# Optimization experiments

Measured on AMD Instinct MI355X. Metric: run time of the kernel, lower is better.

Reference implementation:

```python
import jax, jax.numpy as jnp
import numpy as np

B, T, C = 1, 2048, 2048
N_HEADS, N_KV_HEADS = 32, 8
D_HEAD = C // N_HEADS  # 64
WINDOW = 512
ROPE_BASE = 10000.0


def setup_inputs() -> dict:
    key = jax.random.key(0)
    ks = jax.random.split(key, 5)
    s = 0.02
    return {
        "x": jax.random.normal(ks[0], (B, T, C), dtype=jnp.float32),
        "wq": jax.random.normal(ks[1], (C, N_HEADS * D_HEAD), dtype=jnp.float32) * s,
        "wk": jax.random.normal(ks[2], (C, N_KV_HEADS * D_HEAD), dtype=jnp.float32) * s,
        "wv": jax.random.normal(ks[3], (C, N_KV_HEADS * D_HEAD), dtype=jnp.float32) * s,
        "wo": jax.random.normal(ks[4], (N_HEADS * D_HEAD, C), dtype=jnp.float32) * s,
    }


def _rope_tables(seq_len, d_head, dtype):
    inv_freq = 1.0 / (ROPE_BASE ** (jnp.arange(0, d_head, 2, dtype=jnp.float32) / d_head))
    t = jnp.arange(seq_len, dtype=jnp.float32)
    freqs = t[:, None] * inv_freq[None, :]          # [T, d/2]
    emb = jnp.concatenate([freqs, freqs], axis=-1)  # [T, d]
    return jnp.cos(emb).astype(dtype), jnp.sin(emb).astype(dtype)


def _rotate_half(u):
    d = u.shape[-1]
    return jnp.concatenate([-u[..., d // 2:], u[..., :d // 2]], axis=-1)


def reference(x, wq, wk, wv, wo):
    b, t, c = x.shape
    n_rep = N_HEADS // N_KV_HEADS
    q = (x @ wq).reshape(b, t, N_HEADS, D_HEAD)
    k = (x @ wk).reshape(b, t, N_KV_HEADS, D_HEAD)
    v = (x @ wv).reshape(b, t, N_KV_HEADS, D_HEAD)

    cos, sin = _rope_tables(t, D_HEAD, x.dtype)
    cos = cos[None, :, None, :]
    sin = sin[None, :, None, :]
    q = q * cos + _rotate_half(q) * sin
    k = k * cos + _rotate_half(k) * sin

    # repeat_interleave KV heads up to n_heads (GQA expansion)
    k = jnp.repeat(k, n_rep, axis=2)  # [B,T,H,d]
    v = jnp.repeat(v, n_rep, axis=2)

    scale = 1.0 / np.sqrt(D_HEAD)
    scores = jnp.einsum('bqhd,bkhd->bhqk', q, k) * scale  # [B,H,T,T]

    # sliding-window causal mask: attend iff k<=q and q-k<=window
    qi = jnp.arange(t)[:, None]
    ki = jnp.arange(t)[None, :]
    allowed = (ki <= qi) & (qi - ki <= WINDOW)  # [T,T] bool
    scores = jnp.where(allowed[None, None, :, :], scores, -jnp.inf)

    attn = jax.nn.softmax(scores, axis=-1)
    out = jnp.einsum('bhqk,bkhd->bqhd', attn, v).reshape(b, t, N_HEADS * D_HEAD)
    return out @ wo
```

## Files before the change

### kernel.cpp

```cpp
#include <hip/hip_runtime.h>
#include <hip/hip_bf16.h>
#include <math.h>

#define T_SEQ 2048
#define C_DIM 2048
#define NH    32
#define NKV   8
#define DH    64
#define WIN   512
#define QKV_N 3072

typedef __bf16 bf16x8 __attribute__((ext_vector_type(8)));
typedef __bf16 bf16x4 __attribute__((ext_vector_type(4)));
typedef float  f32x4  __attribute__((ext_vector_type(4)));

__device__ __forceinline__ void gload_lds16(const __bf16* g, __bf16* l) {
  __builtin_amdgcn_global_load_lds(
      (const __attribute__((address_space(1))) void*)g,
      (__attribute__((address_space(3))) void*)l, 16, 0, 0);
}

__device__ __forceinline__ void tr_tile(const float* __restrict__ in,
                                        __bf16* __restrict__ out,
                                        int R, int Ccols, int tile, int tid,
                                        float (*sh)[33]) {
  int tpc = Ccols >> 5;
  int c0 = (tile % tpc) << 5;
  int r0 = (tile / tpc) << 5;
  int tx = tid & 31, ty = tid >> 5;
#pragma unroll
  for (int i = 0; i < 32; i += 8)
    sh[ty + i][tx] = in[(size_t)(r0 + ty + i) * Ccols + c0 + tx];
  __syncthreads();
#pragma unroll
  for (int i = 0; i < 32; i += 8)
    out[(size_t)(c0 + ty + i) * R + r0 + tx] = (__bf16)sh[tx][ty + i];
}

__global__ __launch_bounds__(256) void prep_kernel(
    const float* __restrict__ x, const float* __restrict__ wq,
    const float* __restrict__ wk, const float* __restrict__ wv,
    const float* __restrict__ wo, __bf16* __restrict__ xb,
    __bf16* __restrict__ wqkvT, __bf16* __restrict__ woT,
    float2* __restrict__ tab) {
  __shared__ float sh[32][33];
  int bid = blockIdx.x;
  const int tid = threadIdx.x;
  if (bid < 4096) {
    int i = bid * 256 + tid;
    float4 v = ((const float4*)x)[i];
    bf16x4 o = {(__bf16)v.x, (__bf16)v.y, (__bf16)v.z, (__bf16)v.w};
    *(bf16x4*)(xb + (size_t)i * 4) = o;
    return;
  }
  bid -= 4096;
  if (bid < 256) {
    int i = bid * 256 + tid;
    int j = i & 31, t = i >> 5;
    float inv = powf(10000.0f, -(float)(2 * j) / 64.0f);
    float s, c;
    sincosf((float)t * inv, &s, &c);
    tab[i] = make_float2(c, s);
    return;
  }
  bid -= 256;
  if (bid < 4096) { tr_tile(wq, wqkvT, C_DIM, C_DIM, bid, tid, sh); return; }
  bid -= 4096;
  if (bid < 1024) {
    tr_tile(wk, wqkvT + (size_t)2048 * C_DIM, C_DIM, NKV * DH, bid, tid, sh);
    return;
  }
  bid -= 1024;
  if (bid < 1024) {
    tr_tile(wv, wqkvT + (size_t)2560 * C_DIM, C_DIM, NKV * DH, bid, tid, sh);
    return;
  }
  bid -= 1024;
  tr_tile(wo, woT, C_DIM, C_DIM, bid, tid, sh);
}

template <typename OutT, bool ROPE>
__global__ __launch_bounds__(256) void gemm_bf16_kernel(
    const __bf16* __restrict__ A, const __bf16* __restrict__ Bt,
    OutT* __restrict__ C, const float2* __restrict__ rope_tab,
    int M, int N, int K) {
  __shared__ __bf16 As[2][128 * 64];
  __shared__ __bf16 Bs[2][64 * 64];

  const int tid = threadIdx.x;
  const int wid = tid >> 6, l = tid & 63;
  const int lm = l & 15, lh = l >> 4;
  const int brow = blockIdx.y * 128, bcol = blockIdx.x * 64;

  const int kb_swz = (((l & 7) ^ (l >> 3)) << 3);
  const int srow   = l >> 3;

  f32x4 acc[2][4] = {};
  const int NT = K >> 6;

#pragma unroll
  for (int c = 0; c < 6; ++c) {
    int ci = wid + c * 4;
    if (ci < 16) {
      int row = ci * 8 + srow;
      gload_lds16(A + (size_t)(brow + row) * K + kb_swz, &As[0][ci * 512]);
    } else {
      int row = (ci - 16) * 8 + srow;
      gload_lds16(Bt + (size_t)(bcol + row) * K + kb_swz, &Bs[0][(ci - 16) * 512]);
    }
  }
  __syncthreads();

  for (int t = 0; t < NT; ++t) {
    const int cur = t & 1;
    if (t + 1 < NT) {
      const int k1 = (t + 1) << 6;
#pragma unroll
      for (int c = 0; c < 6; ++c) {
        int ci = wid + c * 4;
        if (ci < 16) {
          int row = ci * 8 + srow;
          gload_lds16(A + (size_t)(brow + row) * K + k1 + kb_swz,
                      &As[cur ^ 1][ci * 512]);
        } else {
          int row = (ci - 16) * 8 + srow;
          gload_lds16(Bt + (size_t)(bcol + row) * K + k1 + kb_swz,
                      &Bs[cur ^ 1][(ci - 16) * 512]);
        }
      }
    }

    const __bf16* as = As[cur];
    const __bf16* bs = Bs[cur];
    const int x7 = lm & 7;
    bf16x8 af[2][2], bfr[4][2];
#pragma unroll
    for (int i = 0; i < 2; ++i)
#pragma unroll
      for (int u = 0; u < 2; ++u)
        af[i][u] = *(const bf16x8*)&as[(wid * 32 + i * 16 + lm) * 64 +
                                       (((u * 4 + lh) ^ x7) << 3)];
#pragma unroll
    for (int j = 0; j < 4; ++j)
#pragma unroll
      for (int u = 0; u < 2; ++u)
        bfr[j][u] = *(const bf16x8*)&bs[(j * 16 + lm) * 64 +
                                        (((u * 4 + lh) ^ x7) << 3)];
#pragma unroll
    for (int u = 0; u < 2; ++u)
#pragma unroll
      for (int i = 0; i < 2; ++i)
#pragma unroll
        for (int j = 0; j < 4; ++j)
          acc[i][j] = __builtin_amdgcn_mfma_f32_16x16x32_bf16(
              af[i][u], bfr[j][u], acc[i][j], 0, 0, 0);

    __syncthreads();
  }

  if (ROPE) {
    if (bcol < 2560) {
#pragma unroll
      for (int i = 0; i < 2; ++i)
#pragma unroll
        for (int r = 0; r < 4; ++r) {
          int t = brow + wid * 32 + i * 16 + lh * 4 + r;
#pragma unroll
          for (int j = 0; j < 2; ++j) {
            float2 cs = rope_tab[t * 32 + j * 16 + lm];
            float v0 = acc[i][j][r], v1 = acc[i][j + 2][r];
            acc[i][j][r]     = v0 * cs.x - v1 * cs.y;
            acc[i][j + 2][r] = v1 * cs.x + v0 * cs.y;
          }
        }
    }
  }

#pragma unroll
  for (int i = 0; i < 2; ++i)
#pragma unroll
    for (int j = 0; j < 4; ++j)
#pragma unroll
      for (int r = 0; r < 4; ++r) {
        int row = brow + wid * 32 + i * 16 + lh * 4 + r;
        int col = bcol + j * 16 + lm;
        C[(size_t)row * N + col] = (OutT)acc[i][j][r];
      }
}

__global__ __launch_bounds__(256) void attn_mfma_kernel(
    const __bf16* __restrict__ QKV, __bf16* __restrict__ O) {
  __shared__ __bf16 K_lds[64][72];
  __shared__ __bf16 Vt[64][72];
  __shared__ __bf16 P_lds[4][16][72];

  const int tid = threadIdx.x;
  const int l   = tid & 63;
  const int w   = tid >> 6;
  const int q0  = blockIdx.x * 64;
  const int h   = blockIdx.y;
  const int kvh = h >> 2;
  const int q0w = q0 + w * 16;
  const int lm  = l & 15;
  const int lh  = l >> 4;

  const __bf16* Qp = QKV + h * DH;
  const __bf16* Kp = QKV + 2048 + kvh * DH;
  const __bf16* Vp = QKV + 2560 + kvh * DH;

  bf16x8 aq0 = *(const bf16x8*)(Qp + (size_t)(q0w + lm) * QKV_N + lh * 8);
  bf16x8 aq1 = *(const bf16x8*)(Qp + (size_t)(q0w + lm) * QKV_N + 32 + lh * 8);

  f32x4 o_acc[4] = {};
  float m[4], lsum[4];
#pragma unroll
  for (int r = 0; r < 4; ++r) { m[r] = -1e30f; lsum[r] = 0.0f; }

  const int klo  = (q0 - WIN) > 0 ? (q0 - WIN) : 0;
  const int skey = tid >> 2;
  const int sdp  = (tid & 3) * 16;

  for (int k0 = klo; k0 < q0 + 64; k0 += 64) {
    __syncthreads();
    {
      const __bf16* ks = Kp + (size_t)(k0 + skey) * QKV_N + sdp;
      *(bf16x8*)&K_lds[skey][sdp]     = *(const bf16x8*)ks;
      *(bf16x8*)&K_lds[skey][sdp + 8] = *(const bf16x8*)(ks + 8);
      const __bf16* vs = Vp + (size_t)(k0 + l) * QKV_N + w * 16;
      bf16x8 v0 = *(const bf16x8*)vs;
      bf16x8 v1 = *(const bf16x8*)(vs + 8);
#pragma unroll
      for (int j = 0; j < 8; ++j) Vt[w * 16 + j][l]     = v0[j];
#pragma unroll
      for (int j = 0; j < 8; ++j) Vt[w * 16 + 8 + j][l] = v1[j];
    }
    __syncthreads();

    f32x4 s[4] = {};
#pragma unroll
    for (int kg = 0; kg < 4; ++kg) {
      bf16x8 kb0 = *(const bf16x8*)&K_lds[kg * 16 + lm][lh * 8];
      bf16x8 kb1 = *(const bf16x8*)&K_lds[kg * 16 + lm][32 + lh * 8];
      s[kg] = __builtin_amdgcn_mfma_f32_16x16x32_bf16(aq0, kb0, s[kg], 0, 0, 0);
      s[kg] = __builtin_amdgcn_mfma_f32_16x16x32_bf16(aq1, kb1, s[kg], 0, 0, 0);
    }

    float sv[4][4];
    float tmax[4] = {-1e30f, -1e30f, -1e30f, -1e30f};
#pragma unroll
    for (int kg = 0; kg < 4; ++kg)
#pragma unroll
      for (int r = 0; r < 4; ++r) {
        int qr = q0w + lh * 4 + r;
        int kc = k0 + kg * 16 + lm;
        float a = s[kg][r] * 0.125f;
        sv[kg][r] = (kc <= qr && kc + WIN >= qr) ? a : -1e30f;
        tmax[r] = fmaxf(tmax[r], sv[kg][r]);
      }
#pragma unroll
    for (int off = 1; off < 16; off <<= 1)
#pragma unroll
      for (int r = 0; r < 4; ++r)
        tmax[r] = fmaxf(tmax[r], __shfl_xor(tmax[r], off));

#pragma unroll
    for (int r = 0; r < 4; ++r) {
      float mn = fmaxf(m[r], tmax[r]);
      float co = __expf(m[r] - mn);
      m[r] = mn;
      float ps = 0.0f;
#pragma unroll
      for (int kg = 0; kg < 4; ++kg) {
        float p = (sv[kg][r] > -1e29f) ? __expf(sv[kg][r] - mn) : 0.0f;
        sv[kg][r] = p;
        ps += p;
      }
#pragma unroll
      for (int off = 1; off < 16; off <<= 1) ps += __shfl_xor(ps, off);
      lsum[r] = lsum[r] * co + ps;
#pragma unroll
      for (int dc = 0; dc < 4; ++dc) o_acc[dc][r] *= co;
    }

#pragma unroll
    for (int kg = 0; kg < 4; ++kg)
#pragma unroll
      for (int r = 0; r < 4; ++r)
        P_lds[w][lh * 4 + r][kg * 16 + lm] = (__bf16)sv[kg][r];
    bf16x8 pf0 = *(const bf16x8*)&P_lds[w][lm][lh * 8];
    bf16x8 pf1 = *(const bf16x8*)&P_lds[w][lm][32 + lh * 8];

#pragma unroll
    for (int dc = 0; dc < 4; ++dc) {
      bf16x8 vb0 = *(const bf16x8*)&Vt[dc * 16 + lm][lh * 8];
      bf16x8 vb1 = *(const bf16x8*)&Vt[dc * 16 + lm][32 + lh * 8];
      o_acc[dc] = __builtin_amdgcn_mfma_f32_16x16x32_bf16(pf0, vb0, o_acc[dc], 0, 0, 0);
      o_acc[dc] = __builtin_amdgcn_mfma_f32_16x16x32_bf16(pf1, vb1, o_acc[dc], 0, 0, 0);
    }
  }

#pragma unroll
  for (int dc = 0; dc < 4; ++dc)
#pragma unroll
    for (int r = 0; r < 4; ++r) {
      int qr = q0w + lh * 4 + r;
      O[(size_t)qr * C_DIM + h * DH + dc * 16 + lm] =
          (__bf16)(o_acc[dc][r] / lsum[r]);
    }
}

extern "C" void kernel_launch(void* const* d_in, const int* in_sizes, int n_in,
                              void* d_out, int out_size, void* d_ws, size_t ws_size,
                              hipStream_t stream) {
  const float* x  = (const float*)d_in[0];
  const float* wq = (const float*)d_in[1];
  const float* wk = (const float*)d_in[2];
  const float* wv = (const float*)d_in[3];
  const float* wo = (const float*)d_in[4];
  float* out = (float*)d_out;

  __bf16* xb    = (__bf16*)d_ws;
  __bf16* wqkvT = xb + (size_t)C_DIM * C_DIM;
  __bf16* woT   = wqkvT + (size_t)QKV_N * C_DIM;
  __bf16* QKV   = woT + (size_t)C_DIM * C_DIM;
  float2* tab   = (float2*)(QKV + (size_t)T_SEQ * QKV_N);
  __bf16* Ab    = xb;

  prep_kernel<<<4096 + 256 + 4096 + 1024 + 1024 + 4096, 256, 0, stream>>>(
      x, wq, wk, wv, wo, xb, wqkvT, woT, tab);

  gemm_bf16_kernel<__bf16, true>
      <<<dim3(QKV_N / 64, T_SEQ / 128), 256, 0, stream>>>(
          xb, wqkvT, QKV, tab, T_SEQ, QKV_N, C_DIM);

  attn_mfma_kernel<<<dim3(T_SEQ / 64, NH), dim3(256), 0, stream>>>(QKV, Ab);

  gemm_bf16_kernel<float, false>
      <<<dim3(C_DIM / 64, T_SEQ / 128), 256, 0, stream>>>(
          Ab, woT, out, nullptr, T_SEQ, C_DIM, C_DIM);
}
```

Baseline: 125.9 us.

## Transpose attention MFMAs, fold softmax scale into Q projection, use exp2

Swaps the MFMA operands so each lane holds a single query row, which removes the cross-lane shuffle reductions per row and lets the output be stored as packed bf16x4. The softmax scale and log2(e) are folded into Q in the projection epilogue so the attention loop can use a raw exp2. Mask evaluation is skipped for tiles lying fully inside the window. The running max now starts at -60, which relies on scores staying above that bound.

```diff
diff --git a/kernel.cpp b/kernel.cpp
--- a/kernel.cpp
+++ b/kernel.cpp
@@ -13,6 +13,12 @@
 typedef __bf16 bf16x8 __attribute__((ext_vector_type(8)));
 typedef __bf16 bf16x4 __attribute__((ext_vector_type(4)));
 typedef float  f32x4  __attribute__((ext_vector_type(4)));
+
+#if __has_builtin(__builtin_amdgcn_exp2f)
+#define EXP2(x) __builtin_amdgcn_exp2f(x)
+#else
+#define EXP2(x) exp2f(x)
+#endif
 
 __device__ __forceinline__ void gload_lds16(const __bf16* g, __bf16* l) {
   __builtin_amdgcn_global_load_lds(
@@ -174,6 +180,14 @@
           }
         }
     }
+    if (bcol < 2048) {
+#pragma unroll
+      for (int i = 0; i < 2; ++i)
+#pragma unroll
+        for (int j = 0; j < 4; ++j)
+#pragma unroll
+          for (int r = 0; r < 4; ++r) acc[i][j][r] *= 0.18033688f;
+    }
   }
 
 #pragma unroll
@@ -212,9 +226,7 @@
   bf16x8 aq1 = *(const bf16x8*)(Qp + (size_t)(q0w + lm) * QKV_N + 32 + lh * 8);
 
   f32x4 o_acc[4] = {};
-  float m[4], lsum[4];
-#pragma unroll
-  for (int r = 0; r < 4; ++r) { m[r] = -1e30f; lsum[r] = 0.0f; }
+  float m = -60.0f, lsum = 0.0f;
 
   const int klo  = (q0 - WIN) > 0 ? (q0 - WIN) : 0;
   const int skey = tid >> 2;
@@ -241,52 +253,61 @@
     for (int kg = 0; kg < 4; ++kg) {
       bf16x8 kb0 = *(const bf16x8*)&K_lds[kg * 16 + lm][lh * 8];
       bf16x8 kb1 = *(const bf16x8*)&K_lds[kg * 16 + lm][32 + lh * 8];
-      s[kg] = __builtin_amdgcn_mfma_f32_16x16x32_bf16(aq0, kb0, s[kg], 0, 0, 0);
-      s[kg] = __builtin_amdgcn_mfma_f32_16x16x32_bf16(aq1, kb1, s[kg], 0, 0, 0);
+      s[kg] = __builtin_amdgcn_mfma_f32_16x16x32_bf16(kb0, aq0, s[kg], 0, 0, 0);
+      s[kg] = __builtin_amdgcn_mfma_f32_16x16x32_bf16(kb1, aq1, s[kg], 0, 0, 0);
     }
 
     float sv[4][4];
-    float tmax[4] = {-1e30f, -1e30f, -1e30f, -1e30f};
+    const bool full = (k0 + 63 <= q0w) && (k0 >= q0w + 15 - WIN);
+    if (full) {
+#pragma unroll
+      for (int kg = 0; kg < 4; ++kg)
+#pragma unroll
+        for (int r = 0; r < 4; ++r) sv[kg][r] = s[kg][r];
+    } else {
+      const int qr = q0w + lm;
+#pragma unroll
+      for (int kg = 0; kg < 4; ++kg)
+#pragma unroll
+        for (int r = 0; r < 4; ++r) {
+          int kc = k0 + kg * 16 + lh * 4 + r;
+          sv[kg][r] = (kc <= qr && kc + WIN >= qr) ? s[kg][r] : -1e30f;
+        }
+    }
+
+    float t01 = fmaxf(fmaxf(fmaxf(sv[0][0], sv[0][1]), fmaxf(sv[0][2], sv[0][3])),
+                      fmaxf(fmaxf(sv[1][0], sv[1][1]), fmaxf(sv[1][2], sv[1][3])));
+    float t23 = fmaxf(fmaxf(fmaxf(sv[2][0], sv[2][1]), fmaxf(sv[2][2], sv[2][3])),
+                      fmaxf(fmaxf(sv[3][0], sv[3][1]), fmaxf(sv[3][2], sv[3][3])));
+    float tmax = fmaxf(t01, t23);
+    tmax = fmaxf(tmax, __shfl_xor(tmax, 16));
+    tmax = fmaxf(tmax, __shfl_xor(tmax, 32));
+
+    float mn = fmaxf(m, tmax);
+    float co = EXP2(m - mn);
+    m = mn;
+    float ps = 0.0f;
 #pragma unroll
     for (int kg = 0; kg < 4; ++kg)
 #pragma unroll
       for (int r = 0; r < 4; ++r) {
-        int qr = q0w + lh * 4 + r;
-        int kc = k0 + kg * 16 + lm;
-        float a = s[kg][r] * 0.125f;
-        sv[kg][r] = (kc <= qr && kc + WIN >= qr) ? a : -1e30f;
-        tmax[r] = fmaxf(tmax[r], sv[kg][r]);
-      }
-#pragma unroll
-    for (int off = 1; off < 16; off <<= 1)
-#pragma unroll
-      for (int r = 0; r < 4; ++r)
-        tmax[r] = fmaxf(tmax[r], __shfl_xor(tmax[r], off));
-
-#pragma unroll
-    for (int r = 0; r < 4; ++r) {
-      float mn = fmaxf(m[r], tmax[r]);
-      float co = __expf(m[r] - mn);
-      m[r] = mn;
-      float ps = 0.0f;
-#pragma unroll
-      for (int kg = 0; kg < 4; ++kg) {
-        float p = (sv[kg][r] > -1e29f) ? __expf(sv[kg][r] - mn) : 0.0f;
+        float p = EXP2(sv[kg][r] - mn);
         sv[kg][r] = p;
         ps += p;
       }
-#pragma unroll
-      for (int off = 1; off < 16; off <<= 1) ps += __shfl_xor(ps, off);
-      lsum[r] = lsum[r] * co + ps;
-#pragma unroll
-      for (int dc = 0; dc < 4; ++dc) o_acc[dc][r] *= co;
-    }
+    ps += __shfl_xor(ps, 16);
+    ps += __shfl_xor(ps, 32);
+    lsum = lsum * co + ps;
+#pragma unroll
+    for (int dc = 0; dc < 4; ++dc)
+#pragma unroll
+      for (int r = 0; r < 4; ++r) o_acc[dc][r] *= co;
 
 #pragma unroll
     for (int kg = 0; kg < 4; ++kg)
 #pragma unroll
       for (int r = 0; r < 4; ++r)
-        P_lds[w][lh * 4 + r][kg * 16 + lm] = (__bf16)sv[kg][r];
+        P_lds[w][lm][kg * 16 + lh * 4 + r] = (__bf16)sv[kg][r];
     bf16x8 pf0 = *(const bf16x8*)&P_lds[w][lm][lh * 8];
     bf16x8 pf1 = *(const bf16x8*)&P_lds[w][lm][32 + lh * 8];
 
@@ -294,19 +315,19 @@
     for (int dc = 0; dc < 4; ++dc) {
       bf16x8 vb0 = *(const bf16x8*)&Vt[dc * 16 + lm][lh * 8];
       bf16x8 vb1 = *(const bf16x8*)&Vt[dc * 16 + lm][32 + lh * 8];
-      o_acc[dc] = __builtin_amdgcn_mfma_f32_16x16x32_bf16(pf0, vb0, o_acc[dc], 0, 0, 0);
-      o_acc[dc] = __builtin_amdgcn_mfma_f32_16x16x32_bf16(pf1, vb1, o_acc[dc], 0, 0, 0);
-    }
-  }
-
-#pragma unroll
-  for (int dc = 0; dc < 4; ++dc)
-#pragma unroll
-    for (int r = 0; r < 4; ++r) {
-      int qr = q0w + lh * 4 + r;
-      O[(size_t)qr * C_DIM + h * DH + dc * 16 + lm] =
-          (__bf16)(o_acc[dc][r] / lsum[r]);
-    }
+      o_acc[dc] = __builtin_amdgcn_mfma_f32_16x16x32_bf16(vb0, pf0, o_acc[dc], 0, 0, 0);
+      o_acc[dc] = __builtin_amdgcn_mfma_f32_16x16x32_bf16(vb1, pf1, o_acc[dc], 0, 0, 0);
+    }
+  }
+
+  const float inv = 1.0f / lsum;
+#pragma unroll
+  for (int dc = 0; dc < 4; ++dc) {
+    bf16x4 ov;
+#pragma unroll
+    for (int r = 0; r < 4; ++r) ov[r] = (__bf16)(o_acc[dc][r] * inv);
+    *(bf16x4*)&O[(size_t)(q0w + lm) * C_DIM + h * DH + dc * 16 + lh * 4] = ov;
+  }
 }
 
 extern "C" void kernel_launch(void* const* d_in, const int* in_sizes, int n_in,
```

New measurement: 114.8 us. 8.8% less time.
